# Kernel optimization log

Hardware: AMD Instinct MI355X
Metric: run time of the kernel (lower is better)

## Reference

```python
import jax, jax.numpy as jnp
import numpy as np

K = 1024  # num_embeddings
D = 256   # embedding_dim
BETA = 0.25
DELTA = 1.0


def setup_inputs() -> dict:
    key = jax.random.key(0)
    k1, k2 = jax.random.split(key)
    latents_mean = jax.random.normal(k1, (64, 1024, D), dtype=jnp.float32)
    # nn.Embedding weight initialized uniform(-1/K, 1/K)
    embedding_weight = jax.random.uniform(
        k2, (K, D), dtype=jnp.float32, minval=-1.0 / K, maxval=1.0 / K
    )
    return {"latents_mean": latents_mean, "embedding_weight": embedding_weight}


def reference(latents_mean, embedding_weight):
    latents_shape = latents_mean.shape
    flat = latents_mean.reshape(-1, D)                      # [N, D]
    dist = (
        jnp.sum(flat ** 2, axis=1, keepdims=True)
        + jnp.sum(embedding_weight ** 2, axis=1)
        - 2.0 * flat @ embedding_weight.T
    )                                                       # [N, K]
    encoding_inds = jnp.argmin(dist, axis=1)                # [N]
    # direct gather (same math as one-hot @ weight)
    quantized = embedding_weight[encoding_inds].reshape(latents_shape)

    commitment_loss = jnp.mean((jax.lax.stop_gradient(quantized) - latents_mean) ** 2)
    embedding_loss = jnp.mean((quantized - jax.lax.stop_gradient(latents_mean)) ** 2)
    vq_loss = commitment_loss * BETA + DELTA * embedding_loss

    # straight-through estimator
    quantized_st = latents_mean + jax.lax.stop_gradient(quantized - latents_mean)

    n = flat.shape[0]
    avg_probs = jnp.zeros((K,), flat.dtype).at[encoding_inds].add(1.0) / n
    perplexity = jnp.exp(-jnp.sum(avg_probs * jnp.log(avg_probs + 1e-10)))

    return quantized_st, vq_loss, perplexity, encoding_inds[:, None], dist
```

## Files before the change

### kernel.cpp

```cpp
#include <hip/hip_runtime.h>

#define NROWS 65536
#define KCODES 1024
#define DDIM 256

#define Q_OFF    0
#define LOSS_OFF 16777216
#define PERP_OFF 16777217
#define IND_OFF  16777218
#define DIST_OFF 16842754

#define MARGIN  1.5e-3f
#define PRUNE   1.5e-3f
#define MAXCAND 16
#define RG_BLOCKS (NROWS / 16)

typedef unsigned long long u64;
typedef unsigned int u32;
typedef unsigned short u16;
typedef __attribute__((ext_vector_type(8))) short bf16x8;
typedef __attribute__((ext_vector_type(4))) float f32x4;

__device__ inline u32 f2bf_bits(float f) {
    u32 u = __float_as_uint(f);
    return (u + 0x7fffu + ((u >> 16) & 1u)) >> 16;
}

__global__ __launch_bounds__(256) void sqnorm_kernel(
    const float* __restrict__ lat, const float* __restrict__ emb,
    float* __restrict__ row_sq, float* __restrict__ emb_sq) {
    int gwave = (blockIdx.x * 256 + threadIdx.x) >> 6;
    int lane = threadIdx.x & 63;
    if (gwave >= NROWS + KCODES) return;
    const float* src = (gwave < NROWS) ? lat + (size_t)gwave * DDIM
                                       : emb + (size_t)(gwave - NROWS) * DDIM;
    float4 v = *reinterpret_cast<const float4*>(src + lane * 4);
    float s = v.x * v.x + v.y * v.y + v.z * v.z + v.w * v.w;
#pragma unroll
    for (int m = 32; m >= 1; m >>= 1) s += __shfl_xor(s, m, 64);
    if (lane == 0) {
        if (gwave < NROWS) row_sq[gwave] = s;
        else emb_sq[gwave - NROWS] = s;
    }
}

__global__ __launch_bounds__(256) void convert_kernel(
    const float* __restrict__ lat, const float* __restrict__ emb,
    u16* __restrict__ Apre, u16* __restrict__ Bpre,
    u32* __restrict__ cand_cnt, u32* __restrict__ hist) {
    const int NA_IT = NROWS * 32;
    const int NB_IT = KCODES * 32;
    int g = blockIdx.x * 256 + threadIdx.x;
    if (g < NROWS) cand_cnt[g] = 0u;
    if (g < KCODES) hist[g] = 0u;
    if (g >= NA_IT + NB_IT) return;
    const float* src;
    uint4* dst;
    int it;
    if (g < NA_IT) { src = lat; dst = (uint4*)Apre; it = g; }
    else           { src = emb; dst = (uint4*)Bpre; it = g - NA_IT; }
    int c = it & 3, ks = (it >> 2) & 7, rg = it >> 5;
    const float* s = src + (size_t)rg * DDIM + ks * 32 + c * 8;
    float4 v0 = *reinterpret_cast<const float4*>(s);
    float4 v1 = *reinterpret_cast<const float4*>(s + 4);
    u32 h0 = f2bf_bits(v0.x), h1 = f2bf_bits(v0.y), h2 = f2bf_bits(v0.z), h3 = f2bf_bits(v0.w);
    u32 h4 = f2bf_bits(v1.x), h5 = f2bf_bits(v1.y), h6 = f2bf_bits(v1.z), h7 = f2bf_bits(v1.w);
    uint4 hq = make_uint4(h0 | (h1 << 16), h2 | (h3 << 16), h4 | (h5 << 16), h6 | (h7 << 16));
    int r = rg & 127, tile = rg >> 7;
    dst[((size_t)(tile * 8 + ks) * 128 + r) * 4 + (c ^ (r & 3))] = hq;
}

__global__ __launch_bounds__(256, 3) void dist_row_kernel(
    const u16* __restrict__ Apre, const u16* __restrict__ Bpre,
    const float* __restrict__ row_sq, const float* __restrict__ emb_sq,
    float* __restrict__ dist, u32* __restrict__ cand_cnt,
    u16* __restrict__ cand, float* __restrict__ cand_dv) {
    __shared__ __align__(16) float tr[8 * 1032];
    __shared__ float rowmin_lds[4][16];
    const int tid = threadIdx.x;
    const int lane = tid & 63, w = tid >> 6;
    const int li = lane & 15, lg = lane >> 4;
    const int row0 = blockIdx.x * 16;
    const int tA = row0 >> 7;
    const int rloc = (row0 & 127) + li;
    const int wcol0 = w * 256;

    f32x4 acc[16];
#pragma unroll
    for (int nf = 0; nf < 16; ++nf) acc[nf] = (f32x4)0.0f;

    const char* Abase = (const char*)Apre + (size_t)tA * 65536;
    const char* Bbase = (const char*)Bpre;

#pragma unroll
    for (int ks = 0; ks < 8; ++ks) {
        bf16x8 af = *reinterpret_cast<const bf16x8*>(
            Abase + ((size_t)(ks * 128 + rloc)) * 64 + ((lg ^ (rloc & 3)) << 4));
#pragma unroll
        for (int g = 0; g < 2; ++g) {
            bf16x8 bf[8];
#pragma unroll
            for (int j = 0; j < 8; ++j) {
                int cc = wcol0 + (g * 8 + j) * 16 + li;
                int tb = cc >> 7, cloc = cc & 127;
                bf[j] = *reinterpret_cast<const bf16x8*>(
                    Bbase + ((size_t)(tb * 8 + ks) * 128 + cloc) * 64 +
                    ((lg ^ (cloc & 3)) << 4));
            }
#pragma unroll
            for (int j = 0; j < 8; ++j)
                acc[g * 8 + j] = __builtin_amdgcn_mfma_f32_16x16x32_bf16(
                    af, bf[j], acc[g * 8 + j], 0, 0, 0);
        }
    }

    float rs_r[4], es16[16];
#pragma unroll
    for (int rg = 0; rg < 4; ++rg) rs_r[rg] = row_sq[row0 + lg * 4 + rg];
#pragma unroll
    for (int nf = 0; nf < 16; ++nf) es16[nf] = emb_sq[wcol0 + nf * 16 + li];

    float rmin[4] = {3.4e38f, 3.4e38f, 3.4e38f, 3.4e38f};
#pragma unroll
    for (int nf = 0; nf < 16; ++nf)
#pragma unroll
        for (int rg = 0; rg < 4; ++rg) {
            float dv = (rs_r[rg] + es16[nf]) - 2.0f * acc[nf][rg];
            rmin[rg] = fminf(rmin[rg], dv);
        }
#pragma unroll
    for (int m = 8; m >= 1; m >>= 1)
#pragma unroll
        for (int rg = 0; rg < 4; ++rg)
            rmin[rg] = fminf(rmin[rg], __shfl_xor(rmin[rg], m, 64));
    if (li == 0) {
#pragma unroll
        for (int rg = 0; rg < 4; ++rg) rowmin_lds[w][lg * 4 + rg] = rmin[rg];
    }
    __syncthreads();
    float rowm[4];
#pragma unroll
    for (int rg = 0; rg < 4; ++rg) {
        float a = fminf(rowmin_lds[0][lg * 4 + rg], rowmin_lds[1][lg * 4 + rg]);
        float b = fminf(rowmin_lds[2][lg * 4 + rg], rowmin_lds[3][lg * 4 + rg]);
        rowm[rg] = fminf(a, b) + MARGIN;
    }

#pragma unroll
    for (int nf = 0; nf < 16; ++nf)
#pragma unroll
        for (int rg = 0; rg < 4; ++rg) {
            float dv = (rs_r[rg] + es16[nf]) - 2.0f * acc[nf][rg];
            if (dv <= rowm[rg]) {
                int grow = row0 + lg * 4 + rg;
                u32 slot = atomicAdd(&cand_cnt[grow], 1u);
                if (slot < MAXCAND) {
                    cand[(size_t)grow * MAXCAND + slot] = (u16)(wcol0 + nf * 16 + li);
                    cand_dv[(size_t)grow * MAXCAND + slot] = dv;
                }
            }
        }

#pragma unroll
    for (int p = 0; p < 2; ++p) {
        __syncthreads();
        if ((lg >> 1) == p) {
#pragma unroll
            for (int nf = 0; nf < 16; ++nf)
#pragma unroll
                for (int rg = 0; rg < 4; ++rg) {
                    float dv = (rs_r[rg] + es16[nf]) - 2.0f * acc[nf][rg];
                    tr[((lg & 1) * 4 + rg) * 1032 + wcol0 + nf * 16 + li] = dv;
                }
        }
        __syncthreads();
#pragma unroll
        for (int rr = 0; rr < 2; ++rr) {
            int r = w * 2 + rr;
#pragma unroll
            for (int it = 0; it < 4; ++it) {
                float4 v = *reinterpret_cast<const float4*>(
                    &tr[r * 1032 + it * 256 + lane * 4]);
                *reinterpret_cast<float4*>(
                    dist + (size_t)(row0 + p * 8 + r) * KCODES + it * 256 + lane * 4) = v;
            }
        }
    }
}

__global__ __launch_bounds__(256) void refine_gather_kernel(
    const float* __restrict__ lat, const float* __restrict__ emb,
    const float* __restrict__ row_sq, const float* __restrict__ emb_sq,
    const u32* __restrict__ cand_cnt, const u16* __restrict__ cand,
    const float* __restrict__ cand_dv,
    float* __restrict__ qout, float* __restrict__ indout,
    u32* __restrict__ hist, float* __restrict__ loss_part) {
    __shared__ __align__(16) float xs[4][4][260];
    __shared__ int bestc_l[16];
    __shared__ float lred[4];
    const int w = threadIdx.x >> 6, lane = threadIdx.x & 63;
    const int rw = lane >> 4, slot = lane & 15;
    const int row0 = blockIdx.x * 16;

#pragma unroll
    for (int rr = 0; rr < 4; ++rr) {
        int row = row0 + w * 4 + rr;
        float4 xv = *reinterpret_cast<const float4*>(lat + (size_t)row * DDIM + lane * 4);
        *reinterpret_cast<float4*>(&xs[w][rr][lane * 4]) = xv;
    }
    __syncthreads();

    const int row = row0 + w * 4 + rw;
    int cntraw = (int)cand_cnt[row];
    int cnt = (cntraw > MAXCAND) ? MAXCAND : cntraw;
    int sl = (slot < cnt) ? slot : 0;
    int c = cand[(size_t)row * MAXCAND + sl];
    float cd = cand_dv[(size_t)row * MAXCAND + sl];

    float cm = cd;
#pragma unroll
    for (int m = 8; m >= 1; m >>= 1) cm = fminf(cm, __shfl_xor(cm, m, 64));
    bool keep = cd <= cm + PRUNE;
    u64 bal = __ballot(keep);
    u32 mask16 = (u32)(bal >> (rw * 16)) & 0xFFFFu;
    int s0 = __ffs(mask16) - 1;
    if (!keep) {
        sl = s0;
        c = cand[(size_t)row * MAXCAND + s0];
    }

    const float* erow = emb + (size_t)c * DDIM;
    float4 e0 = *reinterpret_cast<const float4*>(erow + 0);
    float4 e1 = *reinterpret_cast<const float4*>(erow + 4);
    float4 e2 = *reinterpret_cast<const float4*>(erow + 8);
    float4 e3 = *reinterpret_cast<const float4*>(erow + 12);
    float4 e4 = *reinterpret_cast<const float4*>(erow + 16);
    float4 e5 = *reinterpret_cast<const float4*>(erow + 20);
    float4 e6 = *reinterpret_cast<const float4*>(erow + 24);
    float4 e7 = *reinterpret_cast<const float4*>(erow + 28);
    float acc = 0.0f;
#define STEP(PF, K) { \
        float4 xq = *reinterpret_cast<const float4*>(&xs[w][rw][(K) * 4]); \
        acc = __builtin_fmaf(xq.x, PF.x, acc); \
        acc = __builtin_fmaf(xq.y, PF.y, acc); \
        acc = __builtin_fmaf(xq.z, PF.z, acc); \
        acc = __builtin_fmaf(xq.w, PF.w, acc); \
        if ((K) + 8 < 64) PF = *reinterpret_cast<const float4*>(erow + ((K) + 8) * 4); }
#define GROUP(G) STEP(e0, (G)*8+0) STEP(e1, (G)*8+1) STEP(e2, (G)*8+2) STEP(e3, (G)*8+3) \
                 STEP(e4, (G)*8+4) STEP(e5, (G)*8+5) STEP(e6, (G)*8+6) STEP(e7, (G)*8+7)
    GROUP(0) GROUP(1) GROUP(2) GROUP(3) GROUP(4) GROUP(5) GROUP(6) GROUP(7)
#undef GROUP
#undef STEP
    float t = row_sq[row] + emb_sq[c];
    float dv = __builtin_fmaf(-2.0f, acc, t);

#pragma unroll
    for (int m = 8; m >= 1; m >>= 1) {
        float od = __shfl_xor(dv, m, 64);
        int oc = __shfl_xor(c, m, 64);
        if (od < dv || (od == dv && oc < c)) { dv = od; c = oc; }
    }

    u64 ovm = __ballot(slot == 0 && cntraw > MAXCAND);
    while (ovm) {
        int l = __ffsll((long long)ovm) - 1;
        ovm &= ovm - 1;
        int ow = l >> 4;
        int orow = row0 + w * 4 + ow;
        float tbase = row_sq[orow];
        float bdv = 3.4e38f;
        int bc = KCODES;
        for (int j = 0; j < 16; ++j) {
            int cc = lane + j * 64;
            const float* er = emb + (size_t)cc * DDIM;
            float a2 = 0.0f;
            for (int k4 = 0; k4 < 64; ++k4) {
                float4 ev = *reinterpret_cast<const float4*>(er + k4 * 4);
                float4 xq = *reinterpret_cast<const float4*>(&xs[w][ow][k4 * 4]);
                a2 = __builtin_fmaf(xq.x, ev.x, a2);
                a2 = __builtin_fmaf(xq.y, ev.y, a2);
                a2 = __builtin_fmaf(xq.z, ev.z, a2);
                a2 = __builtin_fmaf(xq.w, ev.w, a2);
            }
            float dv2 = __builtin_fmaf(-2.0f, a2, tbase + emb_sq[cc]);
            if (dv2 < bdv || (dv2 == bdv && cc < bc)) { bdv = dv2; bc = cc; }
        }
#pragma unroll
        for (int m = 32; m >= 1; m >>= 1) {
            float od = __shfl_xor(bdv, m, 64);
            int oc = __shfl_xor(bc, m, 64);
            if (od < bdv || (od == bdv && oc < bc)) { bdv = od; bc = oc; }
        }
        if (rw == ow) { dv = bdv; c = bc; }
    }

    if (slot == 0) {
        bestc_l[w * 4 + rw] = c;
        indout[row] = (float)c;
        atomicAdd(&hist[c], 1u);
    }
    __syncthreads();

    float ssum = 0.0f;
#pragma unroll
    for (int p = 0; p < 4; ++p) {
        int rl = p * 4 + w;
        int grow = row0 + rl;
        int bc = bestc_l[rl];
        float4 xv = *reinterpret_cast<const float4*>(&xs[p][w][lane * 4]);
        float4 ev = *reinterpret_cast<const float4*>(emb + (size_t)bc * DDIM + lane * 4);
        float dx = ev.x - xv.x, dy = ev.y - xv.y, dz = ev.z - xv.z, dw = ev.w - xv.w;
        float4 q = make_float4(xv.x + dx, xv.y + dy, xv.z + dz, xv.w + dw);
        *reinterpret_cast<float4*>(qout + (size_t)grow * DDIM + lane * 4) = q;
        float s = dx * dx + dy * dy + dz * dz + dw * dw;
#pragma unroll
        for (int m = 32; m >= 1; m >>= 1) s += __shfl_xor(s, m, 64);
        ssum += s;
    }
    if (lane == 0) lred[w] = ssum;
    __syncthreads();
    if (threadIdx.x == 0)
        loss_part[blockIdx.x] = (lred[0] + lred[1]) + (lred[2] + lred[3]);
}

__global__ __launch_bounds__(1024) void scalar_kernel(
    const u32* __restrict__ hist, const float* __restrict__ loss_part,
    float* __restrict__ out_loss, float* __restrict__ out_perp) {
    __shared__ double lred[16];
    __shared__ float ered[16];
    int t = threadIdx.x;
    double ls = 0.0;
#pragma unroll
    for (int i = 0; i < RG_BLOCKS / 1024; ++i)
        ls += (double)loss_part[t + i * 1024];
    float p = (float)hist[t] / 65536.0f;
    float es = p * logf(p + 1e-10f);
#pragma unroll
    for (int m = 32; m >= 1; m >>= 1) {
        ls += __shfl_xor(ls, m, 64);
        es += __shfl_xor(es, m, 64);
    }
    if ((t & 63) == 0) { lred[t >> 6] = ls; ered[t >> 6] = es; }
    __syncthreads();
    if (t < 64) {
        double lv = (t < 16) ? lred[t] : 0.0;
        float ev = (t < 16) ? ered[t] : 0.0f;
#pragma unroll
        for (int m = 32; m >= 1; m >>= 1) {
            lv += __shfl_xor(lv, m, 64);
            ev += __shfl_xor(ev, m, 64);
        }
        if (t == 0) {
            *out_perp = expf(-ev);
            double ml = lv / (double)((size_t)NROWS * DDIM);
            *out_loss = (float)(ml * 0.25 + ml);
        }
    }
}

extern "C" void kernel_launch(void* const* d_in, const int* in_sizes, int n_in,
                              void* d_out, int out_size, void* d_ws, size_t ws_size,
                              hipStream_t stream) {
    const float* lat = (const float*)d_in[0];
    const float* emb = (const float*)d_in[1];
    float* out = (float*)d_out;
    char* ws = (char*)d_ws;

    u32* cand_cnt = (u32*)ws;
    u16* cand = (u16*)(ws + 262144);
    float* cand_dv = (float*)(ws + 2359296);
    float* row_sq = (float*)(ws + 6553600);
    float* emb_sq = (float*)(ws + 6815744);
    u32* hist = (u32*)(ws + 6819840);
    float* loss_part = (float*)(ws + 6823936);
    u16* Apre = (u16*)(ws + 6840320);
    u16* Bpre = (u16*)(ws + 40394752);

    sqnorm_kernel<<<(NROWS + KCODES) / 4, 256, 0, stream>>>(lat, emb, row_sq, emb_sq);
    convert_kernel<<<(NROWS * 32 + KCODES * 32) / 256, 256, 0, stream>>>(
        lat, emb, Apre, Bpre, cand_cnt, hist);
    dist_row_kernel<<<4096, 256, 0, stream>>>(Apre, Bpre, row_sq, emb_sq,
                                              out + DIST_OFF, cand_cnt, cand, cand_dv);
    refine_gather_kernel<<<RG_BLOCKS, 256, 0, stream>>>(lat, emb, row_sq, emb_sq,
                                                        cand_cnt, cand, cand_dv,
                                                        out + Q_OFF, out + IND_OFF,
                                                        hist, loss_part);
    scalar_kernel<<<1, 1024, 0, stream>>>(hist, loss_part,
                                          out + LOSS_OFF, out + PERP_OFF);
}
```

Before: 197.1 us.

## Process 32 rows per block in dist kernel to reuse B fragments

Each dist_row_kernel block now computes two 16-row MFMA tiles against the same 1024 codes. Every loaded B fragment feeds two MFMAs, which halves B-matrix global/L2 traffic per row, and the grid shrinks to 2048 blocks. The cost is double the accumulator registers, so the occupancy hint drops from 3 to 2 blocks per CU, and the transpose-store phase now takes four passes. The extra register pressure may cause spills or reduce latency hiding.

```diff
diff --git a/kernel.cpp b/kernel.cpp
--- a/kernel.cpp
+++ b/kernel.cpp
@@ -70,109 +70,131 @@
     dst[((size_t)(tile * 8 + ks) * 128 + r) * 4 + (c ^ (r & 3))] = hq;
 }
 
-__global__ __launch_bounds__(256, 3) void dist_row_kernel(
+__global__ __launch_bounds__(256, 2) void dist_row_kernel(
     const u16* __restrict__ Apre, const u16* __restrict__ Bpre,
     const float* __restrict__ row_sq, const float* __restrict__ emb_sq,
     float* __restrict__ dist, u32* __restrict__ cand_cnt,
     u16* __restrict__ cand, float* __restrict__ cand_dv) {
     __shared__ __align__(16) float tr[8 * 1032];
-    __shared__ float rowmin_lds[4][16];
+    __shared__ float rowmin_lds[4][32];
     const int tid = threadIdx.x;
     const int lane = tid & 63, w = tid >> 6;
     const int li = lane & 15, lg = lane >> 4;
-    const int row0 = blockIdx.x * 16;
+    const int row0 = blockIdx.x * 32;
     const int tA = row0 >> 7;
     const int rloc = (row0 & 127) + li;
     const int wcol0 = w * 256;
 
-    f32x4 acc[16];
-#pragma unroll
-    for (int nf = 0; nf < 16; ++nf) acc[nf] = (f32x4)0.0f;
+    f32x4 acc0[16], acc1[16];
+#pragma unroll
+    for (int j = 0; j < 16; ++j) { acc0[j] = (f32x4)0.0f; acc1[j] = (f32x4)0.0f; }
 
     const char* Abase = (const char*)Apre + (size_t)tA * 65536;
     const char* Bbase = (const char*)Bpre;
 
 #pragma unroll
     for (int ks = 0; ks < 8; ++ks) {
-        bf16x8 af = *reinterpret_cast<const bf16x8*>(
+        bf16x8 af0 = *reinterpret_cast<const bf16x8*>(
             Abase + ((size_t)(ks * 128 + rloc)) * 64 + ((lg ^ (rloc & 3)) << 4));
-#pragma unroll
-        for (int g = 0; g < 2; ++g) {
-            bf16x8 bf[8];
-#pragma unroll
-            for (int j = 0; j < 8; ++j) {
-                int cc = wcol0 + (g * 8 + j) * 16 + li;
-                int tb = cc >> 7, cloc = cc & 127;
-                bf[j] = *reinterpret_cast<const bf16x8*>(
-                    Bbase + ((size_t)(tb * 8 + ks) * 128 + cloc) * 64 +
-                    ((lg ^ (cloc & 3)) << 4));
-            }
-#pragma unroll
-            for (int j = 0; j < 8; ++j)
-                acc[g * 8 + j] = __builtin_amdgcn_mfma_f32_16x16x32_bf16(
-                    af, bf[j], acc[g * 8 + j], 0, 0, 0);
-        }
-    }
-
-    float rs_r[4], es16[16];
-#pragma unroll
-    for (int rg = 0; rg < 4; ++rg) rs_r[rg] = row_sq[row0 + lg * 4 + rg];
-#pragma unroll
-    for (int nf = 0; nf < 16; ++nf) es16[nf] = emb_sq[wcol0 + nf * 16 + li];
-
-    float rmin[4] = {3.4e38f, 3.4e38f, 3.4e38f, 3.4e38f};
-#pragma unroll
-    for (int nf = 0; nf < 16; ++nf)
+        int rloc1 = rloc + 16;
+        bf16x8 af1 = *reinterpret_cast<const bf16x8*>(
+            Abase + ((size_t)(ks * 128 + rloc1)) * 64 + ((lg ^ (rloc1 & 3)) << 4));
+#pragma unroll
+        for (int j = 0; j < 16; ++j) {
+            int cc = wcol0 + j * 16 + li;
+            int tb = cc >> 7, cloc = cc & 127;
+            bf16x8 bf = *reinterpret_cast<const bf16x8*>(
+                Bbase + ((size_t)(tb * 8 + ks) * 128 + cloc) * 64 +
+                ((lg ^ (cloc & 3)) << 4));
+            acc0[j] = __builtin_amdgcn_mfma_f32_16x16x32_bf16(af0, bf, acc0[j], 0, 0, 0);
+            acc1[j] = __builtin_amdgcn_mfma_f32_16x16x32_bf16(af1, bf, acc1[j], 0, 0, 0);
+        }
+    }
+
+    float rs0[4], rs1[4], es16[16];
+#pragma unroll
+    for (int rg = 0; rg < 4; ++rg) {
+        rs0[rg] = row_sq[row0 + lg * 4 + rg];
+        rs1[rg] = row_sq[row0 + 16 + lg * 4 + rg];
+    }
+#pragma unroll
+    for (int j = 0; j < 16; ++j) es16[j] = emb_sq[wcol0 + j * 16 + li];
+
+    float rmin0[4] = {3.4e38f, 3.4e38f, 3.4e38f, 3.4e38f};
+    float rmin1[4] = {3.4e38f, 3.4e38f, 3.4e38f, 3.4e38f};
+#pragma unroll
+    for (int j = 0; j < 16; ++j)
 #pragma unroll
         for (int rg = 0; rg < 4; ++rg) {
-            float dv = (rs_r[rg] + es16[nf]) - 2.0f * acc[nf][rg];
-            rmin[rg] = fminf(rmin[rg], dv);
+            rmin0[rg] = fminf(rmin0[rg], (rs0[rg] + es16[j]) - 2.0f * acc0[j][rg]);
+            rmin1[rg] = fminf(rmin1[rg], (rs1[rg] + es16[j]) - 2.0f * acc1[j][rg]);
         }
 #pragma unroll
     for (int m = 8; m >= 1; m >>= 1)
 #pragma unroll
-        for (int rg = 0; rg < 4; ++rg)
-            rmin[rg] = fminf(rmin[rg], __shfl_xor(rmin[rg], m, 64));
+        for (int rg = 0; rg < 4; ++rg) {
+            rmin0[rg] = fminf(rmin0[rg], __shfl_xor(rmin0[rg], m, 64));
+            rmin1[rg] = fminf(rmin1[rg], __shfl_xor(rmin1[rg], m, 64));
+        }
     if (li == 0) {
 #pragma unroll
-        for (int rg = 0; rg < 4; ++rg) rowmin_lds[w][lg * 4 + rg] = rmin[rg];
+        for (int rg = 0; rg < 4; ++rg) {
+            rowmin_lds[w][lg * 4 + rg] = rmin0[rg];
+            rowmin_lds[w][16 + lg * 4 + rg] = rmin1[rg];
+        }
     }
     __syncthreads();
-    float rowm[4];
+    float rowm0[4], rowm1[4];
 #pragma unroll
     for (int rg = 0; rg < 4; ++rg) {
-        float a = fminf(rowmin_lds[0][lg * 4 + rg], rowmin_lds[1][lg * 4 + rg]);
-        float b = fminf(rowmin_lds[2][lg * 4 + rg], rowmin_lds[3][lg * 4 + rg]);
-        rowm[rg] = fminf(a, b) + MARGIN;
-    }
-
-#pragma unroll
-    for (int nf = 0; nf < 16; ++nf)
+        int rl = lg * 4 + rg;
+        rowm0[rg] = fminf(fminf(rowmin_lds[0][rl], rowmin_lds[1][rl]),
+                          fminf(rowmin_lds[2][rl], rowmin_lds[3][rl])) + MARGIN;
+        rowm1[rg] = fminf(fminf(rowmin_lds[0][16 + rl], rowmin_lds[1][16 + rl]),
+                          fminf(rowmin_lds[2][16 + rl], rowmin_lds[3][16 + rl])) + MARGIN;
+    }
+
+#pragma unroll
+    for (int j = 0; j < 16; ++j)
 #pragma unroll
         for (int rg = 0; rg < 4; ++rg) {
-            float dv = (rs_r[rg] + es16[nf]) - 2.0f * acc[nf][rg];
-            if (dv <= rowm[rg]) {
+            float dv0 = (rs0[rg] + es16[j]) - 2.0f * acc0[j][rg];
+            if (dv0 <= rowm0[rg]) {
                 int grow = row0 + lg * 4 + rg;
                 u32 slot = atomicAdd(&cand_cnt[grow], 1u);
                 if (slot < MAXCAND) {
-                    cand[(size_t)grow * MAXCAND + slot] = (u16)(wcol0 + nf * 16 + li);
-                    cand_dv[(size_t)grow * MAXCAND + slot] = dv;
+                    cand[(size_t)grow * MAXCAND + slot] = (u16)(wcol0 + j * 16 + li);
+                    cand_dv[(size_t)grow * MAXCAND + slot] = dv0;
                 }
             }
-        }
-
-#pragma unroll
-    for (int p = 0; p < 2; ++p) {
+            float dv1 = (rs1[rg] + es16[j]) - 2.0f * acc1[j][rg];
+            if (dv1 <= rowm1[rg]) {
+                int grow = row0 + 16 + lg * 4 + rg;
+                u32 slot = atomicAdd(&cand_cnt[grow], 1u);
+                if (slot < MAXCAND) {
+                    cand[(size_t)grow * MAXCAND + slot] = (u16)(wcol0 + j * 16 + li);
+                    cand_dv[(size_t)grow * MAXCAND + slot] = dv1;
+                }
+            }
+        }
+
+#pragma unroll
+    for (int p = 0; p < 4; ++p) {
         __syncthreads();
-        if ((lg >> 1) == p) {
-#pragma unroll
-            for (int nf = 0; nf < 16; ++nf)
-#pragma unroll
-                for (int rg = 0; rg < 4; ++rg) {
-                    float dv = (rs_r[rg] + es16[nf]) - 2.0f * acc[nf][rg];
-                    tr[((lg & 1) * 4 + rg) * 1032 + wcol0 + nf * 16 + li] = dv;
+#pragma unroll
+        for (int fi = 0; fi < 2; ++fi)
+#pragma unroll
+            for (int rg = 0; rg < 4; ++rg) {
+                int rl = fi * 16 + lg * 4 + rg;
+                if ((rl >> 3) == p) {
+#pragma unroll
+                    for (int j = 0; j < 16; ++j) {
+                        float dv = fi ? (rs1[rg] + es16[j]) - 2.0f * acc1[j][rg]
+                                      : (rs0[rg] + es16[j]) - 2.0f * acc0[j][rg];
+                        tr[(rl & 7) * 1032 + wcol0 + j * 16 + li] = dv;
+                    }
                 }
-        }
+            }
         __syncthreads();
 #pragma unroll
         for (int rr = 0; rr < 2; ++rr) {
@@ -379,7 +401,7 @@
     sqnorm_kernel<<<(NROWS + KCODES) / 4, 256, 0, stream>>>(lat, emb, row_sq, emb_sq);
     convert_kernel<<<(NROWS * 32 + KCODES * 32) / 256, 256, 0, stream>>>(
         lat, emb, Apre, Bpre, cand_cnt, hist);
-    dist_row_kernel<<<4096, 256, 0, stream>>>(Apre, Bpre, row_sq, emb_sq,
+    dist_row_kernel<<<2048, 256, 0, stream>>>(Apre, Bpre, row_sq, emb_sq,
                                               out + DIST_OFF, cand_cnt, cand, cand_dv);
     refine_gather_kernel<<<RG_BLOCKS, 256, 0, stream>>>(lat, emb, row_sq, emb_sq,
                                                         cand_cnt, cand, cand_dv,
```

Measured after the change: 220.3 us. +11.8%, slower.
